# Kernel tuning notes

Hardware: AMD Instinct MI355X
Metric: run time of the kernel (lower is better)

## Reference

```python
import jax, jax.numpy as jnp
import numpy as np

NEG = -100.0  # MaxPlusSemiring.zero
V, E = 50000, 300
B, L = 64, 512
P, M = 200, 7          # num patterns, pattern length
D = M * 2 * P          # diag rows
H, C = 100, 2          # mlp hidden, classes


def setup_inputs() -> dict:
    key = jax.random.key(0)
    ks = jax.random.split(key, 12)
    diags = jax.random.normal(ks[1], (D, E), jnp.float32)
    diags = diags / jnp.linalg.norm(diags, axis=1, keepdims=True)  # normalize() in __init__
    return {
        "docs": jax.random.randint(ks[0], (B, L), 0, V),
        "embeddings": jax.random.normal(ks[2], (V, E), jnp.float32),
        "diags": diags,
        "bias": jax.random.normal(ks[3], (D,), jnp.float32),
        "epsilon": jax.random.normal(ks[4], (P, M - 1), jnp.float32),
        "w1": jax.random.normal(ks[5], (P, H), jnp.float32) * 0.05,
        "b1": jnp.zeros((H,), jnp.float32),
        "w2": jax.random.normal(ks[6], (H, H), jnp.float32) * 0.05,
        "b2": jnp.zeros((H,), jnp.float32),
        "w3": jax.random.normal(ks[7], (H, C), jnp.float32) * 0.05,
        "b3": jnp.zeros((C,), jnp.float32),
    }


def _sopa(docs, embeddings, diags, bias, epsilon, w1, b1, w2, b2, w3, b3):
    # transition scores: semiring.from_float = identity for MaxPlus
    emb = embeddings[docs]                                   # [B,L,E]
    ts = jnp.einsum('ble,de->bld', emb, diags) + bias        # [B,L,D]
    T = ts.reshape(B, L, P, 2, M)                            # [B,L,P,diag,M]

    h0 = jnp.full((B, P, M), NEG, ts.dtype).at[:, :, 0].set(0.0)  # one at start state
    s0 = jnp.full((B, P), NEG, ts.dtype)
    zero_pad = jnp.full((B, P, 1), NEG, ts.dtype)            # semiring.zero
    restart = jnp.zeros((B, P, 1), ts.dtype)                 # semiring.one
    eps = epsilon[None]                                      # eps_scale=0 -> identity; [1,P,M-1]

    def step(carry, x):  # x: [B,P,2,M]
        h, s = carry
        after_eps = jnp.maximum(h, jnp.concatenate([zero_pad, h[:, :, :-1] + eps], axis=2))
        main = jnp.concatenate([restart, after_eps[:, :, :-1] + x[:, :, 1, :-1]], axis=2)
        self_loop = after_eps + x[:, :, 0, :]                # self_loop_scale = 0 (identity)
        h_new = jnp.maximum(main, self_loop)
        s_new = jnp.maximum(s, h_new[:, :, -1])              # end state = M-1 for all patterns
        return (h_new, s_new), None

    (_, scores), _ = jax.lax.scan(step, (h0, s0), jnp.moveaxis(T, 1, 0))

    hidden = jax.nn.relu(scores @ w1 + b1)
    hidden = jax.nn.relu(hidden @ w2 + b2)
    return jax.nn.log_softmax(hidden @ w3 + b3, axis=-1)


def reference(docs, embeddings, diags, bias, epsilon, w1, b1, w2, b2, w3, b3):
    return _sopa(docs, embeddings, diags, bias, epsilon, w1, b1, w2, b2, w3, b3)
```

## Files before the change

kernel.cpp:

```cpp
#include <hip/hip_runtime.h>
#include <stdint.h>

#define NEG (-100.0f)

#define NE 300
#define NB 64
#define NL 512
#define NP 200
#define NH 100

#define KP 320
#define UNITS 40
#define ROWB 640

#define PT 8
#define DT 112
#define DTP 128
#define NTILE 25
#define NBROWS (NTILE*DTP)
#define LC 32
#define NCHUNK 16
#define SCW 36

#define LDS_A   (LC*ROWB)
#define LDS_SC  (DT*SCW*4)
#define LDS_TOTAL (3*LDS_A + 2*LDS_SC)

using f32x4  = __attribute__((ext_vector_type(4))) float;
using f32x16 = __attribute__((ext_vector_type(16))) float;
using bf16x8 = __attribute__((ext_vector_type(8))) __bf16;

#define SBAR()       asm volatile("s_barrier" ::: "memory")
#define WAIT_LGKM0() do { asm volatile("s_waitcnt lgkmcnt(0)" ::: "memory"); \
                          __builtin_amdgcn_sched_barrier(0); } while (0)
#define WAIT_VM(N)   do { asm volatile("s_waitcnt vmcnt(" #N ")" ::: "memory"); \
                          __builtin_amdgcn_sched_barrier(0); } while (0)

static __device__ __forceinline__ void gload16(const void* g, void* l) {
    __builtin_amdgcn_global_load_lds(
        (const __attribute__((address_space(1))) void*)g,
        (__attribute__((address_space(3))) void*)l, 16, 0, 0);
}

static __device__ __forceinline__ uint16_t f2bf(float f) {
    union { float f; uint32_t u; } v; v.f = f;
    return (uint16_t)((v.u + 0x7FFFu + ((v.u >> 16) & 1u)) >> 16);
}

static __device__ __forceinline__ void pin(bf16x8& x) {
    asm volatile("" : "+v"(x));
}

static __device__ __forceinline__ float dpp_shr1(float x) {
    int r = __builtin_amdgcn_update_dpp(0, __float_as_int(x), 0x111, 0xF, 0xF, true);
    return __int_as_float(r);
}

__global__ void prep_kernel(const int* __restrict__ docs,
                            const float* __restrict__ emb,
                            const float* __restrict__ diags,
                            const float* __restrict__ bias,
                            uint16_t* __restrict__ A_ws,
                            uint16_t* __restrict__ B_ws)
{
    int tid = blockIdx.x * blockDim.x + threadIdx.x;
    const int totalA = NB * NL * UNITS;
    const int total  = totalA + NBROWS * UNITS;
    if (tid >= total) return;
    const float* src = nullptr; uint16_t* dst; float extra = 0.0f; int r, j;
    bool valid = true;
    if (tid < totalA) {
        r = tid / UNITS; j = tid - r * UNITS;
        src = emb + (size_t)docs[r] * NE;
        dst = A_ws + (size_t)r * KP;
        extra = 1.0f;
    } else {
        int t2 = tid - totalA;
        r = t2 / UNITS; j = t2 - r * UNITS;
        dst = B_ws + (size_t)r * KP;
        int lr = r & (DTP - 1);
        if (lr < DT) {
            int dr = (r >> 7) * DT + lr;
            src = diags + (size_t)dr * NE;
            extra = bias[dr];
        } else {
            valid = false;
        }
    }
    int jp = j ^ (r & 7);
    union { uint16_t h[8]; uint4 v; } u;
    if (!valid) {
        u.v = uint4{0, 0, 0, 0};
    } else if (j < 37) {
        float4 f0 = *reinterpret_cast<const float4*>(src + j * 8);
        float4 f1 = *reinterpret_cast<const float4*>(src + j * 8 + 4);
        u.h[0] = f2bf(f0.x); u.h[1] = f2bf(f0.y);
        u.h[2] = f2bf(f0.z); u.h[3] = f2bf(f0.w);
        u.h[4] = f2bf(f1.x); u.h[5] = f2bf(f1.y);
        u.h[6] = f2bf(f1.z); u.h[7] = f2bf(f1.w);
    } else if (j == 37) {
        float4 f0 = *reinterpret_cast<const float4*>(src + 296);
        u.h[0] = f2bf(f0.x); u.h[1] = f2bf(f0.y);
        u.h[2] = f2bf(f0.z); u.h[3] = f2bf(f0.w);
        u.h[4] = f2bf(extra); u.h[5] = 0; u.h[6] = 0; u.h[7] = 0;
    } else {
        u.v = uint4{0, 0, 0, 0};
    }
    *reinterpret_cast<uint4*>(dst + (size_t)jp * 8) = u.v;
}

static __device__ __forceinline__ void scan_chunk(const float* __restrict__ sc,
        float& h, float& s, float eps_r, bool is_m0, int i0, int i1)
{
    f32x4 xav[8], xbv[8];
#pragma unroll
    for (int i = 0; i < 8; ++i)
        xav[i] = *reinterpret_cast<const f32x4*>(sc + i0 * SCW + i * 4);
#pragma unroll
    for (int i = 0; i < 8; ++i)
        xbv[i] = *reinterpret_cast<const f32x4*>(sc + i1 * SCW + i * 4);
#pragma unroll
    for (int l = 0; l < LC; ++l) {
        float xa = xav[l >> 2][l & 3];
        float xb = xbv[l >> 2][l & 3];
        float hm1  = dpp_shr1(h);
        float t    = is_m0 ? NEG : (hm1 + eps_r);
        float ae   = fmaxf(h, t);
        float aem1 = dpp_shr1(ae);
        float mn   = is_m0 ? 0.0f : (aem1 + xb);
        h = fmaxf(mn, ae + xa);
        s = fmaxf(s, h);
    }
}

__global__ __launch_bounds__(512) __attribute__((amdgpu_waves_per_eu(2, 2)))
void sopa_kernel(const uint16_t* __restrict__ A_ws,
                 const uint16_t* __restrict__ B_ws,
                 const float* __restrict__ epsilon,
                 float* __restrict__ scores_g)
{
    extern __shared__ char smem[];

    const int blk = blockIdx.x;
    const int bb  = blk / NTILE;
    const int pt  = blk - bb * NTILE;
    const int p0  = pt * PT;

    const int tid  = threadIdx.x;
    const int wave = tid >> 6;
    const int lane = tid & 63;

    if (wave < 4) {
        const int arow  = lane & 31;
        const int khalf = lane >> 5;
        const int col   = wave * 32 + arow;
        const int abase = arow * ROWB;
        const int ax3   = arow & 7;
        const bool wr_ok = col < DT;

        bf16x8 breg[20];
        const uint16_t* Bg = B_ws + ((size_t)pt * DTP + col) * KP;
#pragma unroll
        for (int st = 0; st < 20; ++st) {
            int jp = (st * 2 + khalf) ^ (col & 7);
            breg[st] = *reinterpret_cast<const bf16x8*>(Bg + jp * 8);
            pin(breg[st]);
        }
        SBAR();

        for (int c = 0; c < NCHUNK; ++c) {
            const char* Ab  = smem + (c % 3) * LDS_A;
            float*      scw = (float*)(smem + 3 * LDS_A + (c & 1) * LDS_SC);
            f32x16 acc;
#pragma unroll
            for (int i = 0; i < 16; ++i) acc[i] = 0.0f;
#pragma unroll
            for (int st = 0; st < 20; ++st) {
                int jx = (st * 2 + khalf) ^ ax3;
                bf16x8 av = *reinterpret_cast<const bf16x8*>(Ab + abase + jx * 16);
                acc = __builtin_amdgcn_mfma_f32_32x32x16_bf16(av, breg[st], acc, 0, 0, 0);
            }
            if (wr_ok) {
#pragma unroll
                for (int g = 0; g < 4; ++g) {
                    f32x4 v;
                    v[0] = acc[g * 4 + 0]; v[1] = acc[g * 4 + 1];
                    v[2] = acc[g * 4 + 2]; v[3] = acc[g * 4 + 3];
                    *reinterpret_cast<f32x4*>(scw + col * SCW + g * 8 + khalf * 4) = v;
                }
            }
            WAIT_LGKM0();
            SBAR();
        }
    } else if (wave < 6) {
        const int  q  = lane >> 3;
        const int  mm = lane & 7;
        const int  pl = ((wave == 5) ? 4 : 0) + (q & 3);
        const bool is_m0 = (mm == 0);
        float eps_r = 0.0f;
        if (mm >= 1 && mm <= 6) eps_r = epsilon[(p0 + pl) * 6 + (mm - 1)];
        const int i0 = pl * 14 + mm;
        const int i1 = pl * 14 + 7 + (mm ? mm - 1 : 0);
        float h = is_m0 ? 0.0f : NEG;
        float s = NEG;

        SBAR();
        for (int c = 0; c < NCHUNK; ++c) {
            if (c > 0) {
                const float* scr = (const float*)(smem + 3 * LDS_A + ((c - 1) & 1) * LDS_SC);
                scan_chunk(scr, h, s, eps_r, is_m0, i0, i1);
            }
            SBAR();
        }
        const float* scr = (const float*)(smem + 3 * LDS_A + ((NCHUNK - 1) & 1) * LDS_SC);
        scan_chunk(scr, h, s, eps_r, is_m0, i0, i1);
        if (q < 4 && mm == 6) scores_g[bb * NP + p0 + pl] = s;
    } else {
        const int   wv    = wave & 1;
        const char* a_src = (const char*)(A_ws + (size_t)bb * NL * KP) + wv * 10240 + lane * 16;

#pragma unroll
        for (int i = 0; i < 10; ++i)
            gload16(a_src + i * 1024, smem + wv * 10240 + i * 1024);
#pragma unroll
        for (int i = 0; i < 10; ++i)
            gload16(a_src + LC * ROWB + i * 1024, smem + LDS_A + wv * 10240 + i * 1024);
        WAIT_VM(10);
        SBAR();

        for (int c = 0; c < NCHUNK; ++c) {
            if (c + 2 < NCHUNK) {
                const char* src = a_src + (size_t)(c + 2) * LC * ROWB;
                char*       lb  = smem + ((c + 2) % 3) * LDS_A + wv * 10240;
#pragma unroll
                for (int i = 0; i < 10; ++i)
                    gload16(src + i * 1024, lb + i * 1024);
                WAIT_VM(10);
            } else {
                WAIT_VM(0);
            }
            SBAR();
        }
    }
}

__global__ void mlp_kernel(const float* __restrict__ scores_g,
                           const float* __restrict__ w1, const float* __restrict__ b1,
                           const float* __restrict__ w2, const float* __restrict__ b2,
                           const float* __restrict__ w3, const float* __restrict__ b3,
                           float* __restrict__ out)
{
    __shared__ float sc[NP];
    __shared__ float h1[NH];
    __shared__ float h2[NH];
    int b = blockIdx.x, t = threadIdx.x;
    for (int i = t; i < NP; i += blockDim.x) sc[i] = scores_g[b * NP + i];
    __syncthreads();
    if (t < NH) {
        float acc = b1[t];
#pragma unroll 8
        for (int k = 0; k < NP; ++k) acc += sc[k] * w1[k * NH + t];
        h1[t] = fmaxf(acc, 0.0f);
    }
    __syncthreads();
    if (t < NH) {
        float acc = b2[t];
#pragma unroll 8
        for (int k = 0; k < NH; ++k) acc += h1[k] * w2[k * NH + t];
        h2[t] = fmaxf(acc, 0.0f);
    }
    __syncthreads();
    if (t < 64) {
        float l0 = 0.0f, l1 = 0.0f;
        for (int k = t; k < NH; k += 64) {
            float hv = h2[k];
            l0 += hv * w3[k * 2];
            l1 += hv * w3[k * 2 + 1];
        }
#pragma unroll
        for (int off = 32; off > 0; off >>= 1) {
            l0 += __shfl_down(l0, off);
            l1 += __shfl_down(l1, off);
        }
        if (t == 0) {
            l0 += b3[0]; l1 += b3[1];
            float mx  = fmaxf(l0, l1);
            float lse = mx + logf(expf(l0 - mx) + expf(l1 - mx));
            out[b * 2 + 0] = l0 - lse;
            out[b * 2 + 1] = l1 - lse;
        }
    }
}

extern "C" void kernel_launch(void* const* d_in, const int* in_sizes, int n_in,
                              void* d_out, int out_size, void* d_ws, size_t ws_size,
                              hipStream_t stream)
{
    const int*   docs  = (const int*)  d_in[0];
    const float* emb   = (const float*)d_in[1];
    const float* diags = (const float*)d_in[2];
    const float* bias  = (const float*)d_in[3];
    const float* eps   = (const float*)d_in[4];
    const float* w1 = (const float*)d_in[5];
    const float* b1 = (const float*)d_in[6];
    const float* w2 = (const float*)d_in[7];
    const float* b2 = (const float*)d_in[8];
    const float* w3 = (const float*)d_in[9];
    const float* b3 = (const float*)d_in[10];
    float* out = (float*)d_out;

    char* ws = (char*)d_ws;
    uint16_t* A_ws     = (uint16_t*)ws;
    uint16_t* B_ws     = (uint16_t*)(ws + 20971520);
    float*    scores_g = (float*)   (ws + 20971520 + 2048000);

    {
        int totalUnits = (NB * NL + NBROWS) * UNITS;
        int blocks = (totalUnits + 255) / 256;
        prep_kernel<<<blocks, 256, 0, stream>>>(docs, emb, diags, bias, A_ws, B_ws);
    }

    (void)hipFuncSetAttribute(reinterpret_cast<const void*>(sopa_kernel),
                              hipFuncAttributeMaxDynamicSharedMemorySize, LDS_TOTAL);
    sopa_kernel<<<NB * NTILE, 512, LDS_TOTAL, stream>>>(A_ws, B_ws, eps, scores_g);

    mlp_kernel<<<NB, 128, 0, stream>>>(scores_g, w1, b1, w2, b2, w3, b3, out);
}
```

Before: 264.1 us.

## Shrink A staging to double buffer, raise occupancy, split MFMA accumulators

Cuts the LDS staging ring for the embedding chunks from three buffers to two, so the loader prefetches only one chunk ahead and waits for it to fully land before each barrier. The launch attribute changes from exactly 2 waves per EU to a minimum of 4, aiming to fit more blocks per CU with the smaller LDS footprint. The MFMA chain is split into two independent accumulators that are summed before the store, shortening the dependency chain. The cost is a shallower prefetch, which may expose global-load latency, and tighter register limits that could cause spills with 20 pinned B registers.

```diff
diff --git a/kernel.cpp b/kernel.cpp
--- a/kernel.cpp
+++ b/kernel.cpp
@@ -24,7 +24,7 @@
 
 #define LDS_A   (LC*ROWB)
 #define LDS_SC  (DT*SCW*4)
-#define LDS_TOTAL (3*LDS_A + 2*LDS_SC)
+#define LDS_TOTAL (2*LDS_A + 2*LDS_SC)
 
 using f32x4  = __attribute__((ext_vector_type(4))) float;
 using f32x16 = __attribute__((ext_vector_type(16))) float;
@@ -133,7 +133,7 @@
     }
 }
 
-__global__ __launch_bounds__(512) __attribute__((amdgpu_waves_per_eu(2, 2)))
+__global__ __launch_bounds__(512) __attribute__((amdgpu_waves_per_eu(4)))
 void sopa_kernel(const uint16_t* __restrict__ A_ws,
                  const uint16_t* __restrict__ B_ws,
                  const float* __restrict__ epsilon,
@@ -169,23 +169,28 @@
         SBAR();
 
         for (int c = 0; c < NCHUNK; ++c) {
-            const char* Ab  = smem + (c % 3) * LDS_A;
-            float*      scw = (float*)(smem + 3 * LDS_A + (c & 1) * LDS_SC);
-            f32x16 acc;
-#pragma unroll
-            for (int i = 0; i < 16; ++i) acc[i] = 0.0f;
-#pragma unroll
-            for (int st = 0; st < 20; ++st) {
-                int jx = (st * 2 + khalf) ^ ax3;
-                bf16x8 av = *reinterpret_cast<const bf16x8*>(Ab + abase + jx * 16);
-                acc = __builtin_amdgcn_mfma_f32_32x32x16_bf16(av, breg[st], acc, 0, 0, 0);
+            const char* Ab  = smem + (c & 1) * LDS_A;
+            float*      scw = (float*)(smem + 2 * LDS_A + (c & 1) * LDS_SC);
+            f32x16 acc0, acc1;
+#pragma unroll
+            for (int i = 0; i < 16; ++i) { acc0[i] = 0.0f; acc1[i] = 0.0f; }
+#pragma unroll
+            for (int sp = 0; sp < 10; ++sp) {
+                int jx0 = ((sp * 2) * 2 + khalf) ^ ax3;
+                int jx1 = ((sp * 2 + 1) * 2 + khalf) ^ ax3;
+                bf16x8 av0 = *reinterpret_cast<const bf16x8*>(Ab + abase + jx0 * 16);
+                bf16x8 av1 = *reinterpret_cast<const bf16x8*>(Ab + abase + jx1 * 16);
+                acc0 = __builtin_amdgcn_mfma_f32_32x32x16_bf16(av0, breg[sp * 2],     acc0, 0, 0, 0);
+                acc1 = __builtin_amdgcn_mfma_f32_32x32x16_bf16(av1, breg[sp * 2 + 1], acc1, 0, 0, 0);
             }
             if (wr_ok) {
 #pragma unroll
                 for (int g = 0; g < 4; ++g) {
                     f32x4 v;
-                    v[0] = acc[g * 4 + 0]; v[1] = acc[g * 4 + 1];
-                    v[2] = acc[g * 4 + 2]; v[3] = acc[g * 4 + 3];
+                    v[0] = acc0[g * 4 + 0] + acc1[g * 4 + 0];
+                    v[1] = acc0[g * 4 + 1] + acc1[g * 4 + 1];
+                    v[2] = acc0[g * 4 + 2] + acc1[g * 4 + 2];
+                    v[3] = acc0[g * 4 + 3] + acc1[g * 4 + 3];
                     *reinterpret_cast<f32x4*>(scw + col * SCW + g * 8 + khalf * 4) = v;
                 }
             }
@@ -207,12 +212,12 @@
         SBAR();
         for (int c = 0; c < NCHUNK; ++c) {
             if (c > 0) {
-                const float* scr = (const float*)(smem + 3 * LDS_A + ((c - 1) & 1) * LDS_SC);
+                const float* scr = (const float*)(smem + 2 * LDS_A + ((c - 1) & 1) * LDS_SC);
                 scan_chunk(scr, h, s, eps_r, is_m0, i0, i1);
             }
             SBAR();
         }
-        const float* scr = (const float*)(smem + 3 * LDS_A + ((NCHUNK - 1) & 1) * LDS_SC);
+        const float* scr = (const float*)(smem + 2 * LDS_A + ((NCHUNK - 1) & 1) * LDS_SC);
         scan_chunk(scr, h, s, eps_r, is_m0, i0, i1);
         if (q < 4 && mm == 6) scores_g[bb * NP + p0 + pl] = s;
     } else {
@@ -222,21 +227,16 @@
 #pragma unroll
         for (int i = 0; i < 10; ++i)
             gload16(a_src + i * 1024, smem + wv * 10240 + i * 1024);
-#pragma unroll
-        for (int i = 0; i < 10; ++i)
-            gload16(a_src + LC * ROWB + i * 1024, smem + LDS_A + wv * 10240 + i * 1024);
-        WAIT_VM(10);
+        WAIT_VM(0);
         SBAR();
 
         for (int c = 0; c < NCHUNK; ++c) {
-            if (c + 2 < NCHUNK) {
-                const char* src = a_src + (size_t)(c + 2) * LC * ROWB;
-                char*       lb  = smem + ((c + 2) % 3) * LDS_A + wv * 10240;
+            if (c + 1 < NCHUNK) {
+                const char* src = a_src + (size_t)(c + 1) * LC * ROWB;
+                char*       lb  = smem + ((c + 1) & 1) * LDS_A + wv * 10240;
 #pragma unroll
                 for (int i = 0; i < 10; ++i)
                     gload16(src + i * 1024, lb + i * 1024);
-                WAIT_VM(10);
-            } else {
                 WAIT_VM(0);
             }
             SBAR();
```

Result: slower. 324.1 us (+22.7%).
